# Kernel tuning notes

Hardware: AMD Instinct MI355X
Metric: run time of the kernel (lower is better)

The kernel has to match this reference:

```python
import jax, jax.numpy as jnp
import numpy as np

B, S, V, E, H, NL, DFF = 16, 16, 64, 64, 8, 4, 2048
L = S * V
DH = E // H
NUM_GRIDS = 100
POI_DIM = 8
OV_DIM = 8


def setup_inputs() -> dict:
    key = jax.random.key(0)
    ks = jax.random.split(key, 32)
    sc = 0.05
    inp = {}
    inp['features'] = jax.random.normal(ks[0], (B, S, V, 3), jnp.float32)
    inp['overlap_tag'] = jax.random.randint(ks[1], (B, S, V), 0, 3)
    inp['poi_id'] = jax.random.randint(ks[2], (B, S, V), 0, NUM_GRIDS + 1)
    # embedders
    inp['W_raw'] = jax.random.normal(ks[3], (3, E), jnp.float32) * sc
    inp['b_raw'] = jnp.zeros((E,), jnp.float32)
    inp['pos_tab'] = jax.random.normal(ks[4], (S, E), jnp.float32) * sc
    inp['type_tab'] = jax.random.normal(ks[5], (V, E), jnp.float32) * sc
    inp['poi_tab'] = jax.random.normal(ks[6], (NUM_GRIDS + 1, POI_DIM), jnp.float32) * sc
    inp['overlap_tab'] = jax.random.normal(ks[7], (3, OV_DIM), jnp.float32) * sc
    inp['W_comb'] = jax.random.normal(ks[8], (E + OV_DIM + POI_DIM, E), jnp.float32) * sc
    inp['b_comb'] = jnp.zeros((E,), jnp.float32)
    # transformer layers (stacked over NL)
    inp['Wqkv'] = jax.random.normal(ks[9], (NL, E, 3 * E), jnp.float32) * sc
    inp['bqkv'] = jnp.zeros((NL, 3 * E), jnp.float32)
    inp['Wo'] = jax.random.normal(ks[10], (NL, E, E), jnp.float32) * sc
    inp['bo'] = jnp.zeros((NL, E), jnp.float32)
    inp['ln1_s'] = jnp.ones((NL, E), jnp.float32)
    inp['ln1_b'] = jnp.zeros((NL, E), jnp.float32)
    inp['W1'] = jax.random.normal(ks[11], (NL, E, DFF), jnp.float32) * sc
    inp['b1'] = jnp.zeros((NL, DFF), jnp.float32)
    inp['W2'] = jax.random.normal(ks[12], (NL, DFF, E), jnp.float32) * sc
    inp['b2'] = jnp.zeros((NL, E), jnp.float32)
    inp['ln2_s'] = jnp.ones((NL, E), jnp.float32)
    inp['ln2_b'] = jnp.zeros((NL, E), jnp.float32)
    inp['W_head'] = jax.random.normal(ks[13], (E, 3), jnp.float32) * sc
    inp['b_head'] = jnp.zeros((3,), jnp.float32)
    return inp


def _layer_norm(x, s, b):
    m = x.mean(-1, keepdims=True)
    v = ((x - m) ** 2).mean(-1, keepdims=True)
    return (x - m) / jnp.sqrt(v + 1e-5) * s + b


def _forward(features, overlap_tag, poi_id, W_raw, b_raw, pos_tab, type_tab,
             poi_tab, overlap_tab, W_comb, b_comb, Wqkv, bqkv, Wo, bo,
             ln1_s, ln1_b, W1, b1, W2, b2, ln2_s, ln2_b, W_head, b_head):
    # padding_idx=0 rows are zero (as in nn.Embedding(padding_idx=0))
    poi_tab = poi_tab.at[0].set(0.0)
    overlap_tab = overlap_tab.at[0].set(0.0)

    zero_mask = (features.sum(-1) == 0).reshape(B, L)  # [B, L]
    ov_idx = jnp.maximum(overlap_tag, 0)
    poi_idx = jnp.maximum(poi_id, 0)

    feat_e = features @ W_raw + b_raw                    # [B,S,V,E]
    concat = jnp.concatenate([feat_e, overlap_tab[ov_idx], poi_tab[poi_idx]], axis=-1)
    x = (concat @ W_comb + b_comb).reshape(B, L, E)      # [B,L,E]

    t_idx = jnp.repeat(jnp.arange(S), V)                 # [L]
    v_idx = jnp.tile(jnp.arange(V), S)                   # [L]
    struct_mask = (t_idx[:, None] != t_idx[None, :]) & (v_idx[:, None] != v_idx[None, :])
    full_mask = struct_mask[None] | zero_mask[:, None, :] | zero_mask[:, :, None]  # [B,L,L]
    bias = jnp.where(full_mask, -jnp.inf, 0.0)[:, None, :, :]  # [B,1,L,L]

    x = x + pos_tab[t_idx][None] + type_tab[v_idx][None]

    scale = 1.0 / jnp.sqrt(jnp.asarray(DH, x.dtype))
    for l in range(NL):
        qkv = x @ Wqkv[l] + bqkv[l]                      # [B,L,3E]
        q, k, v = jnp.split(qkv, 3, axis=-1)
        q = q.reshape(B, L, H, DH)
        k = k.reshape(B, L, H, DH)
        v = v.reshape(B, L, H, DH)
        scores = jnp.einsum('bqhd,bkhd->bhqk', q, k) * scale + bias
        attn = jax.nn.softmax(scores, axis=-1)
        o = jnp.einsum('bhqk,bkhd->bqhd', attn, v).reshape(B, L, E)
        x = _layer_norm(x + o @ Wo[l] + bo[l], ln1_s[l], ln1_b[l])
        ff = jax.nn.relu(x @ W1[l] + b1[l]) @ W2[l] + b2[l]
        x = _layer_norm(x + ff, ln2_s[l], ln2_b[l])

    last = x.reshape(B, S, V, E)[:, -1]                  # [B,V,E]
    return last @ W_head + b_head                        # [B,V,3]


def reference(features, overlap_tag, poi_id, W_raw, b_raw, pos_tab, type_tab,
              poi_tab, overlap_tab, W_comb, b_comb, Wqkv, bqkv, Wo, bo,
              ln1_s, ln1_b, W1, b1, W2, b2, ln2_s, ln2_b, W_head, b_head):
    return _forward(features, overlap_tag, poi_id, W_raw, b_raw, pos_tab, type_tab,
                    poi_tab, overlap_tab, W_comb, b_comb, Wqkv, bqkv, Wo, bo,
                    ln1_s, ln1_b, W1, b1, W2, b2, ln2_s, ln2_b, W_head, b_head)
```

## Files before the change

kernel.cpp:

```cpp
#include <hip/hip_runtime.h>
#include <math.h>

#define BB 16
#define SS 16
#define VVV 64
#define EE 64
#define HHH 8
#define NLAYER 4
#define DFF_ 2048
#define LL 1024
#define BL 16384
#define PERL 131072

typedef __attribute__((ext_vector_type(8))) _Float16 half8;
typedef __attribute__((ext_vector_type(4))) _Float16 half4v;
typedef __attribute__((ext_vector_type(2))) _Float16 half2v;
typedef __attribute__((ext_vector_type(4))) float f32x4;

#if defined(__has_builtin)
#if __has_builtin(__builtin_amdgcn_fdot2)
#define HAVE_FDOT2 1
#endif
#endif

#define SW64(m, k)  (((m) << 6) + ((((k) >> 3) ^ ((m) & 7)) << 3) + ((k) & 7))


__global__ __launch_bounds__(256) void k_prep(
    const float* __restrict__ W1, const float* __restrict__ W2,
    const float* __restrict__ Wqkv, const float* __restrict__ Wo,
    const float* __restrict__ Wcomb,
    _Float16* __restrict__ w1f, _Float16* __restrict__ w2f,
    _Float16* __restrict__ wqkvf, _Float16* __restrict__ wof,
    _Float16* __restrict__ wcombt)
{
  __shared__ float t[64 * 65];
  int bx = blockIdx.x;
  int cc = threadIdx.x & 63, rr = threadIdx.x >> 6;

  if (bx >= 272) {
    int r0 = (bx - 272) * 64;
#pragma unroll
    for (int i = 0; i < 16; i++) {
      int r = i * 4 + rr;
      if (r0 + r < 80) t[r * 65 + cc] = Wcomb[(size_t)(r0 + r) * 64 + cc];
    }
    __syncthreads();
#pragma unroll
    for (int i = 0; i < 16; i++) {
      int c = i * 4 + rr;
      if (r0 + c < 80) wcombt[(size_t)cc * 80 + r0 + c] = (_Float16)t[c * 65 + cc];
    }
    return;
  }

  const float* src; _Float16* dst; int astr;
  if (bx < 128) {
    int l = bx >> 5, g = bx & 31;
    src = W1 + (size_t)l * PERL + g * 64; astr = 2048;
    dst = w1f + (size_t)(l * 32 + g) * 4096;
  } else if (bx < 256) {
    int j = bx - 128; int l = j >> 5, g = j & 31;
    src = W2 + (size_t)l * PERL + (size_t)g * 64 * 64; astr = 64;
    dst = w2f + (size_t)(l * 32 + g) * 4096;
  } else if (bx < 268) {
    int j = bx - 256; int l = j / 3, g = j % 3;
    src = Wqkv + (size_t)l * 64 * 192 + g * 64; astr = 192;
    dst = wqkvf + (size_t)(l * 3 + g) * 4096;
  } else {
    int l = bx - 268;
    src = Wo + (size_t)l * 4096; astr = 64;
    dst = wof + (size_t)l * 4096;
  }
#pragma unroll
  for (int i = 0; i < 16; i++) {
    int a = i * 4 + rr;
    t[cc * 65 + a] = src[(size_t)a * astr + cc];
  }
  __syncthreads();
#pragma unroll
  for (int it = 0; it < 2; it++) {
    int c = threadIdx.x + it * 256;
    int frag = c >> 6, lane = c & 63;
    int m = (frag >> 1) * 16 + (lane & 15);
    int k0 = (frag & 1) * 32 + (lane >> 4) * 8;
    const float* tr = &t[m * 65 + k0];
    half8 h;
#pragma unroll
    for (int j = 0; j < 8; j++) h[j] = (_Float16)tr[j];
    *(half8*)&dst[(size_t)c * 8] = h;
  }
}

__device__ __forceinline__ void qkv_nb(
    const half8 af[2][2], const _Float16* __restrict__ wqkvf,
    const float* __restrict__ bqkv, _Float16* __restrict__ qbuf,
    _Float16* __restrict__ kbuf, _Float16* __restrict__ vbuf,
    int bx, int nb, int wm, int wn, int lane)
{
  int quad = lane >> 4, l15 = lane & 15;
  const _Float16* bt = wqkvf + (size_t)nb * 4096;
  half8 bf[2][2];
#pragma unroll
  for (int nt = 0; nt < 2; nt++)
#pragma unroll
    for (int ks = 0; ks < 2; ks++)
      bf[nt][ks] = *(const half8*)&bt[(size_t)(((wn * 2 + nt) * 2 + ks) * 512) +
                                      lane * 8];
  f32x4 acc[2][2];
#pragma unroll
  for (int mt = 0; mt < 2; mt++)
#pragma unroll
    for (int nt = 0; nt < 2; nt++) {
      float bv = bqkv[nb * 64 + wn * 32 + nt * 16 + l15];
      acc[mt][nt] = (f32x4){bv, bv, bv, bv};
    }
#pragma unroll
  for (int ks = 0; ks < 2; ks++)
#pragma unroll
    for (int mt = 0; mt < 2; mt++)
#pragma unroll
      for (int nt = 0; nt < 2; nt++)
        acc[mt][nt] = __builtin_amdgcn_mfma_f32_16x16x32_f16(
            af[mt][ks], bf[nt][ks], acc[mt][nt], 0, 0, 0);
#pragma unroll
  for (int mt = 0; mt < 2; mt++)
#pragma unroll
    for (int nt = 0; nt < 2; nt++) {
      int col = wn * 32 + nt * 16 + l15;
#pragma unroll
      for (int r = 0; r < 4; r++) {
        int row = bx * 64 + wm * 32 + mt * 16 + quad * 4 + r;
        _Float16 v = (_Float16)acc[mt][nt][r];
        if (nb == 0) {
          qbuf[(size_t)row * 64 + col] = v;
        } else {
          _Float16* dst = (nb == 1) ? kbuf : vbuf;
          int h = col >> 3, d = col & 7;
          int b = row >> 10, rb = row & 1023;
          dst[((size_t)(b * 8 + h) * 1024 + rb) * 8 + d] = v;
        }
      }
    }
}

__global__ __launch_bounds__(256) void k_embqkv(
    const float* __restrict__ features, const int* __restrict__ ovtag,
    const int* __restrict__ poiid, const float* __restrict__ W_raw,
    const float* __restrict__ b_raw, const float* __restrict__ ov_tab,
    const float* __restrict__ poi_tab, const _Float16* __restrict__ wcombt,
    const float* __restrict__ b_comb, const float* __restrict__ pos_tab,
    const float* __restrict__ type_tab, float* __restrict__ x1,
    float* __restrict__ zm, const _Float16* __restrict__ wqkvf,
    const float* __restrict__ bqkv, _Float16* __restrict__ qbuf,
    _Float16* __restrict__ kbuf, _Float16* __restrict__ vbuf)
{
  constexpr int KP = 104;
  __shared__ _Float16 As[64 * KP];
  __shared__ _Float16 Bs[64 * KP];
  __shared__ _Float16 xs[4096];
  int tid = threadIdx.x;
  int bx = blockIdx.x;
  int m0 = bx * 64;
  int wave = tid >> 6, lane = tid & 63, quad = lane >> 4, l15 = lane & 15;
  int wm = wave >> 1, wn = wave & 1;
  for (int p = tid; p < 1536; p += 256) {
    int r = p / 24, s = p - r * 24; int c = s * 4;
    int row = m0 + r;
    float f0 = features[row * 3 + 0];
    float f1 = features[row * 3 + 1];
    float f2 = features[row * 3 + 2];
    if (s == 0) zm[row] = ((f0 + f1 + f2) == 0.f) ? 1.f : 0.f;
    half4v h;
#pragma unroll
    for (int j = 0; j < 4; j++) {
      int cc = c + j; float v;
      if (cc < 64) {
        v = b_raw[cc] + f0 * W_raw[cc] + f1 * W_raw[64 + cc] + f2 * W_raw[128 + cc];
      } else if (cc < 72) {
        int tt = ovtag[row]; v = (tt <= 0) ? 0.f : ov_tab[tt * 8 + cc - 64];
      } else if (cc < 80) {
        int tt = poiid[row]; v = (tt <= 0) ? 0.f : poi_tab[tt * 8 + cc - 72];
      } else v = 0.f;
      h[j] = (_Float16)v;
    }
    *(half4v*)&As[r * KP + c] = h;
  }
  for (int p = tid; p < 1536; p += 256) {
    int r = p / 24, s = p - r * 24; int c = s * 4;
    half4v h = (half4v){0, 0, 0, 0};
    if (c < 80) h = *(const half4v*)&wcombt[r * 80 + c];
    *(half4v*)&Bs[r * KP + c] = h;
  }
  __syncthreads();
  f32x4 acc[2][2];
#pragma unroll
  for (int mt = 0; mt < 2; mt++)
#pragma unroll
    for (int nt = 0; nt < 2; nt++) {
      float bv = b_comb[wn * 32 + nt * 16 + l15];
      acc[mt][nt] = (f32x4){bv, bv, bv, bv};
    }
#pragma unroll
  for (int ks = 0; ks < 3; ks++) {
    half8 af[2], bf[2];
#pragma unroll
    for (int mt = 0; mt < 2; mt++)
      af[mt] = *(const half8*)&As[(wm * 32 + mt * 16 + l15) * KP + ks * 32 + quad * 8];
#pragma unroll
    for (int nt = 0; nt < 2; nt++)
      bf[nt] = *(const half8*)&Bs[(wn * 32 + nt * 16 + l15) * KP + ks * 32 + quad * 8];
#pragma unroll
    for (int mt = 0; mt < 2; mt++)
#pragma unroll
      for (int nt = 0; nt < 2; nt++)
        acc[mt][nt] = __builtin_amdgcn_mfma_f32_16x16x32_f16(af[mt], bf[nt],
                                                             acc[mt][nt], 0, 0, 0);
  }
#pragma unroll
  for (int mt = 0; mt < 2; mt++)
#pragma unroll
    for (int nt = 0; nt < 2; nt++)
#pragma unroll
      for (int r = 0; r < 4; r++) {
        int lrow = wm * 32 + mt * 16 + quad * 4 + r;
        int row = m0 + lrow;
        int col = wn * 32 + nt * 16 + l15;
        int l = row & (LL - 1);
        float v = acc[mt][nt][r] +
            pos_tab[(l >> 6) * 64 + col] + type_tab[(l & 63) * 64 + col];
        x1[(size_t)row * 64 + col] = v;
        xs[SW64(lrow, col)] = (_Float16)v;
      }
  __syncthreads();
  half8 af[2][2];
#pragma unroll
  for (int mt = 0; mt < 2; mt++)
#pragma unroll
    for (int ks = 0; ks < 2; ks++)
      af[mt][ks] = *(const half8*)&xs[SW64(wm * 32 + mt * 16 + l15,
                                           ks * 32 + quad * 8)];
  for (int nb = 0; nb < 3; nb++)
    qkv_nb(af, wqkvf, bqkv, qbuf, kbuf, vbuf, bx, nb, wm, wn, lane);
}

__global__ __launch_bounds__(256) void k_attn2(
    const _Float16* __restrict__ qbuf, const _Float16* __restrict__ kbuf,
    const _Float16* __restrict__ vbuf, const float* __restrict__ zm,
    _Float16* __restrict__ obuf)
{
  __shared__ _Float16 Ks[1024 * 8];
  __shared__ _Float16 Vs[1024 * 8];
  __shared__ float zs[1024];
  int blk = blockIdx.x;
  int qb = blk & 3, h = (blk >> 2) & 7, b = blk >> 5;
  const _Float16* kb = kbuf + (size_t)(b * 8 + h) * 8192;
  const _Float16* vb = vbuf + (size_t)(b * 8 + h) * 8192;
  for (int p = threadIdx.x; p < 1024; p += 256) {
    *(half8*)&Ks[p * 8] = *(const half8*)&kb[p * 8];
    *(half8*)&Vs[p * 8] = *(const half8*)&vb[p * 8];
    zs[p] = zm[b * LL + p];
  }
  __syncthreads();
  int qrow = qb * 256 + threadIdx.x;
  int tq = qrow >> 6, vq = qrow & 63;
  half8 qh = *(const half8*)&qbuf[(size_t)(b * LL + qrow) * 64 + h * 8];
  const float scale = 0.3535533905932738f;
  float m = -INFINITY, lsum = 0.f;
  float acc[8] = {0.f, 0.f, 0.f, 0.f, 0.f, 0.f, 0.f, 0.f};
  bool zmq = (zs[qrow] != 0.f);

  auto attend = [&](int k) {
    if (zs[k] != 0.f) return;
    half8 kk = *(const half8*)&Ks[k * 8];
    float s = 0.f;
#ifdef HAVE_FDOT2
#pragma unroll
    for (int j = 0; j < 4; j++) {
      half2v qa = (half2v){qh[2 * j], qh[2 * j + 1]};
      half2v ka = (half2v){kk[2 * j], kk[2 * j + 1]};
      s = __builtin_amdgcn_fdot2(qa, ka, s, false);
    }
#else
#pragma unroll
    for (int j = 0; j < 8; j++) s += (float)qh[j] * (float)kk[j];
#endif
    s *= scale;
    half8 vv = *(const half8*)&Vs[k * 8];
    if (s <= m) {
      float p = __expf(s - m);
      lsum += p;
#pragma unroll
      for (int d = 0; d < 8; d++) acc[d] += p * (float)vv[d];
    } else {
      float r = __expf(m - s);
      lsum = lsum * r + 1.f;
#pragma unroll
      for (int d = 0; d < 8; d++) acc[d] = acc[d] * r + (float)vv[d];
      m = s;
    }
  };

  if (!zmq) {
    for (int vv = 0; vv < 64; vv++) attend(tq * 64 + vv);
    for (int tt = 0; tt < 16; tt++) {
      if (tt == tq) continue;
      attend(tt * 64 + vq);
    }
  }
  float inv = 1.f / lsum;
  half8 o;
#pragma unroll
  for (int d = 0; d < 8; d++) o[d] = (_Float16)(acc[d] * inv);
  size_t tile = (size_t)(b * 16 + (qrow >> 6));
  int frag = ((qrow >> 4) & 3) * 2 + (h >> 2);
  int flane = (h & 3) * 16 + (qrow & 15);
  *(half8*)&obuf[tile * 4096 + frag * 512 + flane * 8] = o;
}

__global__ __launch_bounds__(512) void k_layer(
    const _Float16* __restrict__ obuf, const _Float16* __restrict__ wof,
    const float* __restrict__ bo, float* __restrict__ x1,
    const float* __restrict__ ln1_s, const float* __restrict__ ln1_b,
    const _Float16* __restrict__ w1f, const _Float16* __restrict__ w2f,
    const float* __restrict__ b1, const float* __restrict__ b2,
    const float* __restrict__ ln2_s, const float* __restrict__ ln2_b,
    const _Float16* __restrict__ wqkvf, const float* __restrict__ bqkv,
    _Float16* __restrict__ qbuf, _Float16* __restrict__ kbuf,
    _Float16* __restrict__ vbuf, int doqkv)
{
  __shared__ float ots[64 * 68];
  __shared__ _Float16 xs[4096];
  __shared__ float x2f[4096];
  __shared__ _Float16 hs[2][2][4096];
  int tid = threadIdx.x;
  int bx = blockIdx.x;
  int wave = tid >> 6, lane = tid & 63;
  int quad = lane >> 4, l15 = lane & 15;
  int grp = wave >> 2, w4 = wave & 3;
  int wm = w4 >> 1, wn = w4 & 1;

  {
    const _Float16* ot = obuf + (size_t)bx * 4096;
    int mq = grp * 2 + wm;
    half8 af[2], bf[2][2];
#pragma unroll
    for (int ks = 0; ks < 2; ks++)
      af[ks] = *(const half8*)&ot[(size_t)((mq * 2 + ks) * 512) + lane * 8];
#pragma unroll
    for (int nt = 0; nt < 2; nt++)
#pragma unroll
      for (int ks = 0; ks < 2; ks++)
        bf[nt][ks] = *(const half8*)&wof[(size_t)(((wn * 2 + nt) * 2 + ks) * 512) +
                                         lane * 8];
    f32x4 acc[2];
#pragma unroll
    for (int nt = 0; nt < 2; nt++) {
      float bv = bo[wn * 32 + nt * 16 + l15];
      acc[nt] = (f32x4){bv, bv, bv, bv};
    }
#pragma unroll
    for (int ks = 0; ks < 2; ks++)
#pragma unroll
      for (int nt = 0; nt < 2; nt++)
        acc[nt] = __builtin_amdgcn_mfma_f32_16x16x32_f16(af[ks], bf[nt][ks],
                                                         acc[nt], 0, 0, 0);
#pragma unroll
    for (int nt = 0; nt < 2; nt++)
#pragma unroll
      for (int r = 0; r < 4; r++)
        ots[(mq * 16 + quad * 4 + r) * 68 + wn * 32 + nt * 16 + l15] = acc[nt][r];
  }
  __syncthreads();
  for (int i = 0; i < 8; i++) {
    int row = wave * 8 + i;
    size_t off = (size_t)(bx * 64 + row) * 64 + lane;
    float val = ots[row * 68 + lane] + x1[off];
    float sum = val;
#pragma unroll
    for (int o = 32; o > 0; o >>= 1) sum += __shfl_xor(sum, o);
    float mean = sum * (1.f / 64.f);
    float d = val - mean;
    float sq = d * d;
#pragma unroll
    for (int o = 32; o > 0; o >>= 1) sq += __shfl_xor(sq, o);
    float xv = d * rsqrtf(sq * (1.f / 64.f) + 1e-5f) * ln1_s[lane] + ln1_b[lane];
    x2f[row * 64 + lane] = xv;
    xs[SW64(row, lane)] = (_Float16)xv;
  }
  __syncthreads();

  half8 xb[2][2];
#pragma unroll
  for (int mt = 0; mt < 2; mt++)
#pragma unroll
    for (int ks = 0; ks < 2; ks++)
      xb[mt][ks] = *(const half8*)&xs[SW64(wn * 32 + mt * 16 + l15,
                                           ks * 32 + quad * 8)];
  f32x4 acc[2][2];
#pragma unroll
  for (int mt = 0; mt < 2; mt++)
#pragma unroll
    for (int nt = 0; nt < 2; nt++) {
      float bv = (grp == 0) ? b2[wn * 32 + nt * 16 + l15] : 0.f;
      acc[mt][nt] = (f32x4){bv, bv, bv, bv};
    }
  half8 a1[2][2][2], b2w[2][2][2];
  auto loadw = [&](int st, int g) {
    const _Float16* w1t_ = w1f + (size_t)g * 4096;
    const _Float16* w2t_ = w2f + (size_t)g * 4096;
#pragma unroll
    for (int ht = 0; ht < 2; ht++)
#pragma unroll
      for (int ks = 0; ks < 2; ks++)
        a1[st][ht][ks] = *(const half8*)&w1t_[(size_t)(((wm * 2 + ht) * 2 + ks) * 512) +
                                              lane * 8];
#pragma unroll
    for (int nt = 0; nt < 2; nt++)
#pragma unroll
      for (int ks = 0; ks < 2; ks++)
        b2w[st][nt][ks] = *(const half8*)&w2t_[(size_t)(((wn * 2 + nt) * 2 + ks) * 512) +
                                               lane * 8];
  };
  loadw(0, grp);
  for (int i = 0; i < 16; i++) {
    int cur = i & 1;
    if (i < 15) loadw(cur ^ 1, (i + 1) * 2 + grp);
    int g = i * 2 + grp;
    f32x4 hacc[2][2];
#pragma unroll
    for (int ht = 0; ht < 2; ht++)
#pragma unroll
      for (int mt = 0; mt < 2; mt++) hacc[ht][mt] = (f32x4){0.f, 0.f, 0.f, 0.f};
#pragma unroll
    for (int ks = 0; ks < 2; ks++)
#pragma unroll
      for (int ht = 0; ht < 2; ht++)
#pragma unroll
        for (int mt = 0; mt < 2; mt++)
          hacc[ht][mt] = __builtin_amdgcn_mfma_f32_16x16x32_f16(
              a1[cur][ht][ks], xb[mt][ks], hacc[ht][mt], 0, 0, 0);
#pragma unroll
    for (int ht = 0; ht < 2; ht++) {
      float4 bb = *(const float4*)&b1[g * 64 + wm * 32 + ht * 16 + quad * 4];
#pragma unroll
      for (int mt = 0; mt < 2; mt++) {
        f32x4 hv = hacc[ht][mt];
        half4v hp = (half4v){
            (_Float16)fmaxf(hv[0] + bb.x, 0.f), (_Float16)fmaxf(hv[1] + bb.y, 0.f),
            (_Float16)fmaxf(hv[2] + bb.z, 0.f), (_Float16)fmaxf(hv[3] + bb.w, 0.f)};
        *(half4v*)&hs[grp][cur][SW64(wn * 32 + mt * 16 + l15,
                                     wm * 32 + ht * 16 + quad * 4)] = hp;
      }
    }
    __syncthreads();
#pragma unroll
    for (int ks = 0; ks < 2; ks++)
#pragma unroll
      for (int mt = 0; mt < 2; mt++) {
        half8 a2 = *(const half8*)&hs[grp][cur][SW64(wm * 32 + mt * 16 + l15,
                                                     ks * 32 + quad * 8)];
#pragma unroll
        for (int nt = 0; nt < 2; nt++)
          acc[mt][nt] = __builtin_amdgcn_mfma_f32_16x16x32_f16(a2, b2w[cur][nt][ks],
                                                               acc[mt][nt], 0, 0, 0);
      }
  }
  __syncthreads();
  if (grp == 0) {
#pragma unroll
    for (int mt = 0; mt < 2; mt++)
#pragma unroll
      for (int nt = 0; nt < 2; nt++)
#pragma unroll
        for (int r = 0; r < 4; r++)
          ots[(wm * 32 + mt * 16 + quad * 4 + r) * 68 + wn * 32 + nt * 16 + l15] =
              acc[mt][nt][r];
  }
  __syncthreads();
  if (grp == 1) {
#pragma unroll
    for (int mt = 0; mt < 2; mt++)
#pragma unroll
      for (int nt = 0; nt < 2; nt++)
#pragma unroll
        for (int r = 0; r < 4; r++)
          ots[(wm * 32 + mt * 16 + quad * 4 + r) * 68 + wn * 32 + nt * 16 + l15] +=
              acc[mt][nt][r];
  }
  __syncthreads();
  for (int i = 0; i < 8; i++) {
    int row = wave * 8 + i;
    size_t off = (size_t)(bx * 64 + row) * 64 + lane;
    float val = ots[row * 68 + lane] + x2f[row * 64 + lane];
    float sum = val;
#pragma unroll
    for (int o = 32; o > 0; o >>= 1) sum += __shfl_xor(sum, o);
    float mean = sum * (1.f / 64.f);
    float d = val - mean;
    float sq = d * d;
#pragma unroll
    for (int o = 32; o > 0; o >>= 1) sq += __shfl_xor(sq, o);
    float xv = d * rsqrtf(sq * (1.f / 64.f) + 1e-5f) * ln2_s[lane] + ln2_b[lane];
    x1[off] = xv;
    xs[SW64(row, lane)] = (_Float16)xv;
  }
  if (!doqkv) return;
  __syncthreads();
  half8 af[2][2];
#pragma unroll
  for (int mt = 0; mt < 2; mt++)
#pragma unroll
    for (int ks = 0; ks < 2; ks++)
      af[mt][ks] = *(const half8*)&xs[SW64(wm * 32 + mt * 16 + l15,
                                           ks * 32 + quad * 8)];
  for (int nb = grp; nb < 3; nb += 2)
    qkv_nb(af, wqkvf, bqkv, qbuf, kbuf, vbuf, bx, nb, wm, wn, lane);
}

__global__ __launch_bounds__(256) void k_head(
    const float* __restrict__ x, const float* __restrict__ Wh,
    const float* __restrict__ bh, float* __restrict__ out)
{
  int id = blockIdx.x * 256 + threadIdx.x;
  int b = id >> 6, v = id & 63;
  const float* xr = x + (size_t)(b * LL + (SS - 1) * VVV + v) * 64;
  float a0 = bh[0], a1 = bh[1], a2 = bh[2];
  for (int e = 0; e < 64; e++) {
    float xv = xr[e];
    a0 += xv * Wh[e * 3 + 0];
    a1 += xv * Wh[e * 3 + 1];
    a2 += xv * Wh[e * 3 + 2];
  }
  out[id * 3 + 0] = a0;
  out[id * 3 + 1] = a1;
  out[id * 3 + 2] = a2;
}

extern "C" void kernel_launch(void* const* d_in, const int* in_sizes, int n_in,
                              void* d_out, int out_size, void* d_ws, size_t ws_size,
                              hipStream_t stream) {
  const float* features = (const float*)d_in[0];
  const int*   ovtag    = (const int*)d_in[1];
  const int*   poiid    = (const int*)d_in[2];
  const float* W_raw    = (const float*)d_in[3];
  const float* b_raw    = (const float*)d_in[4];
  const float* pos_tab  = (const float*)d_in[5];
  const float* type_tab = (const float*)d_in[6];
  const float* poi_tab  = (const float*)d_in[7];
  const float* ov_tab   = (const float*)d_in[8];
  const float* W_comb   = (const float*)d_in[9];
  const float* b_comb   = (const float*)d_in[10];
  const float* Wqkv     = (const float*)d_in[11];
  const float* bqkv     = (const float*)d_in[12];
  const float* Wo       = (const float*)d_in[13];
  const float* bo       = (const float*)d_in[14];
  const float* ln1_s    = (const float*)d_in[15];
  const float* ln1_b    = (const float*)d_in[16];
  const float* W1       = (const float*)d_in[17];
  const float* b1       = (const float*)d_in[18];
  const float* W2       = (const float*)d_in[19];
  const float* b2       = (const float*)d_in[20];
  const float* ln2_s    = (const float*)d_in[21];
  const float* ln2_b    = (const float*)d_in[22];
  const float* W_head   = (const float*)d_in[23];
  const float* b_head   = (const float*)d_in[24];
  float* out = (float*)d_out;
  float* ws  = (float*)d_ws;

  float* zm  = ws;
  float* x1  = zm + BL;
  _Float16* qbuf   = (_Float16*)(x1 + (size_t)BL * 64);
  _Float16* kbuf   = qbuf + (size_t)BL * 64;
  _Float16* vbuf   = kbuf + (size_t)BL * 64;
  _Float16* obuf16 = vbuf + (size_t)BL * 64;
  _Float16* wcombt = obuf16 + (size_t)BL * 64;
  _Float16* w1f    = wcombt + 5120;
  _Float16* w2f    = w1f + (size_t)NLAYER * PERL;
  _Float16* wqkvf  = w2f + (size_t)NLAYER * PERL;
  _Float16* wof    = wqkvf + (size_t)NLAYER * 3 * 4096;

  k_prep<<<274, 256, 0, stream>>>(W1, W2, Wqkv, Wo, W_comb,
                                  w1f, w2f, wqkvf, wof, wcombt);
  k_embqkv<<<256, 256, 0, stream>>>(features, ovtag, poiid, W_raw, b_raw,
                                    ov_tab, poi_tab, wcombt, b_comb,
                                    pos_tab, type_tab, x1, zm,
                                    wqkvf, bqkv, qbuf, kbuf, vbuf);
  for (int l = 0; l < NLAYER; l++) {
    k_attn2<<<512, 256, 0, stream>>>(qbuf, kbuf, vbuf, zm, obuf16);
    int doqkv = (l < NLAYER - 1);
    k_layer<<<256, 512, 0, stream>>>(
        obuf16, wof + (size_t)l * 4096, bo + l * EE, x1,
        ln1_s + l * EE, ln1_b + l * EE,
        w1f + (size_t)l * PERL, w2f + (size_t)l * PERL,
        b1 + l * DFF_, b2 + l * EE,
        ln2_s + l * EE, ln2_b + l * EE,
        wqkvf + (size_t)(l + 1) * 3 * 4096, bqkv + (l + 1) * 192,
        qbuf, kbuf, vbuf, doqkv);
  }
  k_head<<<4, 256, 0, stream>>>(x1, W_head, b_head, out);
}
```

Baseline: 311.6 us.

## Fuse head into last layer, restructure FFN double buffering, unify Q layout

Removes the separate head kernel: the final layer kernel keeps normalized rows in shared memory, and the blocks that own the last time step compute the 3-way output projection directly. The FFN loop is rewritten as an explicitly unrolled two-stage ping-pong using named register buffers instead of indexed arrays, which is meant to keep the buffers in registers rather than scratch. Q is now written in the same head-major layout as K and V, so attention reads one contiguous half8 per query, and that load is issued before the K/V staging. This saves a launch and simplifies the stores, but the head projection runs serially on a few threads in a handful of blocks.

```diff
diff --git a/kernel.cpp b/kernel.cpp
--- a/kernel.cpp
+++ b/kernel.cpp
@@ -93,7 +93,7 @@
 }
 
 __device__ __forceinline__ void qkv_nb(
-    const half8 af[2][2], const _Float16* __restrict__ wqkvf,
+    const half8 (&af)[2][2], const _Float16* __restrict__ wqkvf,
     const float* __restrict__ bqkv, _Float16* __restrict__ qbuf,
     _Float16* __restrict__ kbuf, _Float16* __restrict__ vbuf,
     int bx, int nb, int wm, int wn, int lane)
@@ -123,24 +123,85 @@
       for (int nt = 0; nt < 2; nt++)
         acc[mt][nt] = __builtin_amdgcn_mfma_f32_16x16x32_f16(
             af[mt][ks], bf[nt][ks], acc[mt][nt], 0, 0, 0);
+  _Float16* dst = (nb == 0) ? qbuf : ((nb == 1) ? kbuf : vbuf);
 #pragma unroll
   for (int mt = 0; mt < 2; mt++)
 #pragma unroll
     for (int nt = 0; nt < 2; nt++) {
       int col = wn * 32 + nt * 16 + l15;
+      int h = col >> 3, d = col & 7;
 #pragma unroll
       for (int r = 0; r < 4; r++) {
         int row = bx * 64 + wm * 32 + mt * 16 + quad * 4 + r;
-        _Float16 v = (_Float16)acc[mt][nt][r];
-        if (nb == 0) {
-          qbuf[(size_t)row * 64 + col] = v;
-        } else {
-          _Float16* dst = (nb == 1) ? kbuf : vbuf;
-          int h = col >> 3, d = col & 7;
-          int b = row >> 10, rb = row & 1023;
-          dst[((size_t)(b * 8 + h) * 1024 + rb) * 8 + d] = v;
-        }
+        int b = row >> 10, rb = row & 1023;
+        dst[((size_t)(b * 8 + h) * 1024 + rb) * 8 + d] = (_Float16)acc[mt][nt][r];
       }
+    }
+}
+
+__device__ __forceinline__ void ffn_load(
+    const _Float16* __restrict__ w1f, const _Float16* __restrict__ w2f, int g,
+    half8 (&a1)[2][2], half8 (&b2w)[2][2], int wm, int wn, int lane)
+{
+  const _Float16* w1t_ = w1f + (size_t)g * 4096;
+  const _Float16* w2t_ = w2f + (size_t)g * 4096;
+#pragma unroll
+  for (int ht = 0; ht < 2; ht++)
+#pragma unroll
+    for (int ks = 0; ks < 2; ks++)
+      a1[ht][ks] = *(const half8*)&w1t_[(size_t)(((wm * 2 + ht) * 2 + ks) * 512) +
+                                        lane * 8];
+#pragma unroll
+  for (int nt = 0; nt < 2; nt++)
+#pragma unroll
+    for (int ks = 0; ks < 2; ks++)
+      b2w[nt][ks] = *(const half8*)&w2t_[(size_t)(((wn * 2 + nt) * 2 + ks) * 512) +
+                                         lane * 8];
+}
+
+__device__ __forceinline__ void ffn_step(
+    const half8 (&a1)[2][2], const half8 (&b2w)[2][2], const half8 (&xb)[2][2],
+    _Float16* hsbuf, const float* __restrict__ b1, int g, f32x4 (&acc)[2][2],
+    int wm, int wn, int lane)
+{
+  int quad = lane >> 4, l15 = lane & 15;
+  f32x4 hacc[2][2];
+#pragma unroll
+  for (int ht = 0; ht < 2; ht++)
+#pragma unroll
+    for (int mt = 0; mt < 2; mt++) hacc[ht][mt] = (f32x4){0.f, 0.f, 0.f, 0.f};
+#pragma unroll
+  for (int ks = 0; ks < 2; ks++)
+#pragma unroll
+    for (int ht = 0; ht < 2; ht++)
+#pragma unroll
+      for (int mt = 0; mt < 2; mt++)
+        hacc[ht][mt] = __builtin_amdgcn_mfma_f32_16x16x32_f16(
+            a1[ht][ks], xb[mt][ks], hacc[ht][mt], 0, 0, 0);
+#pragma unroll
+  for (int ht = 0; ht < 2; ht++) {
+    float4 bb = *(const float4*)&b1[g * 64 + wm * 32 + ht * 16 + quad * 4];
+#pragma unroll
+    for (int mt = 0; mt < 2; mt++) {
+      f32x4 hv = hacc[ht][mt];
+      half4v hp = (half4v){
+          (_Float16)fmaxf(hv[0] + bb.x, 0.f), (_Float16)fmaxf(hv[1] + bb.y, 0.f),
+          (_Float16)fmaxf(hv[2] + bb.z, 0.f), (_Float16)fmaxf(hv[3] + bb.w, 0.f)};
+      *(half4v*)&hsbuf[SW64(wn * 32 + mt * 16 + l15,
+                            wm * 32 + ht * 16 + quad * 4)] = hp;
+    }
+  }
+  __syncthreads();
+#pragma unroll
+  for (int ks = 0; ks < 2; ks++)
+#pragma unroll
+    for (int mt = 0; mt < 2; mt++) {
+      half8 a2 = *(const half8*)&hsbuf[SW64(wm * 32 + mt * 16 + l15,
+                                            ks * 32 + quad * 8)];
+#pragma unroll
+      for (int nt = 0; nt < 2; nt++)
+        acc[mt][nt] = __builtin_amdgcn_mfma_f32_16x16x32_f16(a2, b2w[nt][ks],
+                                                             acc[mt][nt], 0, 0, 0);
     }
 }
 
@@ -254,6 +315,8 @@
   __shared__ float zs[1024];
   int blk = blockIdx.x;
   int qb = blk & 3, h = (blk >> 2) & 7, b = blk >> 5;
+  int qrow = qb * 256 + threadIdx.x;
+  half8 qh = *(const half8*)&qbuf[(size_t)(b * 8 + h) * 8192 + (size_t)qrow * 8];
   const _Float16* kb = kbuf + (size_t)(b * 8 + h) * 8192;
   const _Float16* vb = vbuf + (size_t)(b * 8 + h) * 8192;
   for (int p = threadIdx.x; p < 1024; p += 256) {
@@ -262,9 +325,7 @@
     zs[p] = zm[b * LL + p];
   }
   __syncthreads();
-  int qrow = qb * 256 + threadIdx.x;
   int tq = qrow >> 6, vq = qrow & 63;
-  half8 qh = *(const half8*)&qbuf[(size_t)(b * LL + qrow) * 64 + h * 8];
   const float scale = 0.3535533905932738f;
   float m = -INFINITY, lsum = 0.f;
   float acc[8] = {0.f, 0.f, 0.f, 0.f, 0.f, 0.f, 0.f, 0.f};
@@ -327,7 +388,9 @@
     const float* __restrict__ ln2_s, const float* __restrict__ ln2_b,
     const _Float16* __restrict__ wqkvf, const float* __restrict__ bqkv,
     _Float16* __restrict__ qbuf, _Float16* __restrict__ kbuf,
-    _Float16* __restrict__ vbuf, int doqkv)
+    _Float16* __restrict__ vbuf, int doqkv,
+    const float* __restrict__ Wh, const float* __restrict__ bh,
+    float* __restrict__ out)
 {
   __shared__ float ots[64 * 68];
   __shared__ _Float16 xs[4096];
@@ -405,66 +468,13 @@
       float bv = (grp == 0) ? b2[wn * 32 + nt * 16 + l15] : 0.f;
       acc[mt][nt] = (f32x4){bv, bv, bv, bv};
     }
-  half8 a1[2][2][2], b2w[2][2][2];
-  auto loadw = [&](int st, int g) {
-    const _Float16* w1t_ = w1f + (size_t)g * 4096;
-    const _Float16* w2t_ = w2f + (size_t)g * 4096;
-#pragma unroll
-    for (int ht = 0; ht < 2; ht++)
-#pragma unroll
-      for (int ks = 0; ks < 2; ks++)
-        a1[st][ht][ks] = *(const half8*)&w1t_[(size_t)(((wm * 2 + ht) * 2 + ks) * 512) +
-                                              lane * 8];
-#pragma unroll
-    for (int nt = 0; nt < 2; nt++)
-#pragma unroll
-      for (int ks = 0; ks < 2; ks++)
-        b2w[st][nt][ks] = *(const half8*)&w2t_[(size_t)(((wn * 2 + nt) * 2 + ks) * 512) +
-                                               lane * 8];
-  };
-  loadw(0, grp);
-  for (int i = 0; i < 16; i++) {
-    int cur = i & 1;
-    if (i < 15) loadw(cur ^ 1, (i + 1) * 2 + grp);
-    int g = i * 2 + grp;
-    f32x4 hacc[2][2];
-#pragma unroll
-    for (int ht = 0; ht < 2; ht++)
-#pragma unroll
-      for (int mt = 0; mt < 2; mt++) hacc[ht][mt] = (f32x4){0.f, 0.f, 0.f, 0.f};
-#pragma unroll
-    for (int ks = 0; ks < 2; ks++)
-#pragma unroll
-      for (int ht = 0; ht < 2; ht++)
-#pragma unroll
-        for (int mt = 0; mt < 2; mt++)
-          hacc[ht][mt] = __builtin_amdgcn_mfma_f32_16x16x32_f16(
-              a1[cur][ht][ks], xb[mt][ks], hacc[ht][mt], 0, 0, 0);
-#pragma unroll
-    for (int ht = 0; ht < 2; ht++) {
-      float4 bb = *(const float4*)&b1[g * 64 + wm * 32 + ht * 16 + quad * 4];
-#pragma unroll
-      for (int mt = 0; mt < 2; mt++) {
-        f32x4 hv = hacc[ht][mt];
-        half4v hp = (half4v){
-            (_Float16)fmaxf(hv[0] + bb.x, 0.f), (_Float16)fmaxf(hv[1] + bb.y, 0.f),
-            (_Float16)fmaxf(hv[2] + bb.z, 0.f), (_Float16)fmaxf(hv[3] + bb.w, 0.f)};
-        *(half4v*)&hs[grp][cur][SW64(wn * 32 + mt * 16 + l15,
-                                     wm * 32 + ht * 16 + quad * 4)] = hp;
-      }
-    }
-    __syncthreads();
-#pragma unroll
-    for (int ks = 0; ks < 2; ks++)
-#pragma unroll
-      for (int mt = 0; mt < 2; mt++) {
-        half8 a2 = *(const half8*)&hs[grp][cur][SW64(wm * 32 + mt * 16 + l15,
-                                                     ks * 32 + quad * 8)];
-#pragma unroll
-        for (int nt = 0; nt < 2; nt++)
-          acc[mt][nt] = __builtin_amdgcn_mfma_f32_16x16x32_f16(a2, b2w[cur][nt][ks],
-                                                               acc[mt][nt], 0, 0, 0);
-      }
+  half8 a1x[2][2], b2x[2][2], a1y[2][2], b2y[2][2];
+  ffn_load(w1f, w2f, grp, a1x, b2x, wm, wn, lane);
+  for (int ii = 0; ii < 8; ii++) {
+    ffn_load(w1f, w2f, ii * 4 + 2 + grp, a1y, b2y, wm, wn, lane);
+    ffn_step(a1x, b2x, xb, &hs[grp][0][0], b1, ii * 4 + grp, acc, wm, wn, lane);
+    if (ii < 7) ffn_load(w1f, w2f, ii * 4 + 4 + grp, a1x, b2x, wm, wn, lane);
+    ffn_step(a1y, b2y, xb, &hs[grp][1][0], b1, ii * 4 + 2 + grp, acc, wm, wn, lane);
   }
   __syncthreads();
   if (grp == 0) {
@@ -503,9 +513,21 @@
     for (int o = 32; o > 0; o >>= 1) sq += __shfl_xor(sq, o);
     float xv = d * rsqrtf(sq * (1.f / 64.f) + 1e-5f) * ln2_s[lane] + ln2_b[lane];
     x1[off] = xv;
+    x2f[row * 64 + lane] = xv;
     xs[SW64(row, lane)] = (_Float16)xv;
   }
-  if (!doqkv) return;
+  if (!doqkv) {
+    __syncthreads();
+    if ((bx & 15) == 15 && tid < 192) {
+      int b = bx >> 4;
+      int v = tid / 3, j = tid - v * 3;
+      float a = bh[j];
+      for (int e = 0; e < 64; e++)
+        a += x2f[v * 64 + e] * Wh[e * 3 + j];
+      out[((size_t)(b * 64 + v)) * 3 + j] = a;
+    }
+    return;
+  }
   __syncthreads();
   half8 af[2][2];
 #pragma unroll
@@ -516,25 +538,6 @@
                                            ks * 32 + quad * 8)];
   for (int nb = grp; nb < 3; nb += 2)
     qkv_nb(af, wqkvf, bqkv, qbuf, kbuf, vbuf, bx, nb, wm, wn, lane);
-}
-
-__global__ __launch_bounds__(256) void k_head(
-    const float* __restrict__ x, const float* __restrict__ Wh,
-    const float* __restrict__ bh, float* __restrict__ out)
-{
-  int id = blockIdx.x * 256 + threadIdx.x;
-  int b = id >> 6, v = id & 63;
-  const float* xr = x + (size_t)(b * LL + (SS - 1) * VVV + v) * 64;
-  float a0 = bh[0], a1 = bh[1], a2 = bh[2];
-  for (int e = 0; e < 64; e++) {
-    float xv = xr[e];
-    a0 += xv * Wh[e * 3 + 0];
-    a1 += xv * Wh[e * 3 + 1];
-    a2 += xv * Wh[e * 3 + 2];
-  }
-  out[id * 3 + 0] = a0;
-  out[id * 3 + 1] = a1;
-  out[id * 3 + 2] = a2;
 }
 
 extern "C" void kernel_launch(void* const* d_in, const int* in_sizes, int n_in,
@@ -595,8 +598,8 @@
         w1f + (size_t)l * PERL, w2f + (size_t)l * PERL,
         b1 + l * DFF_, b2 + l * EE,
         ln2_s + l * EE, ln2_b + l * EE,
-        wqkvf + (size_t)(l + 1) * 3 * 4096, bqkv + (l + 1) * 192,
-        qbuf, kbuf, vbuf, doqkv);
-  }
-  k_head<<<4, 256, 0, stream>>>(x1, W_head, b_head, out);
-}
+        wqkvf + (size_t)(l + 1 < NLAYER ? l + 1 : 0) * 3 * 4096,
+        bqkv + (l + 1 < NLAYER ? l + 1 : 0) * 192,
+        qbuf, kbuf, vbuf, doqkv, W_head, b_head, out);
+  }
+}
```

Result: no change. 317.4 us (+1.9%).
